# Kernel tuning notes

Measured on AMD Instinct MI355X. Metric: run time of the kernel, lower is better.

Reference implementation:

```python
import jax, jax.numpy as jnp
import numpy as np


def _relative_position_index(ws):
    # matches SpatialAttention.build with qWh=qWw=kWh=kWw=ws
    coords = np.stack(np.meshgrid(np.arange(ws), np.arange(ws), indexing='ij'))
    cf = coords.reshape(2, -1)  # [2, N]
    rel = (cf[:, :, None] - cf[:, None, :]).transpose(1, 2, 0)  # [N, N, 2]
    rel[:, :, 0] += ws - 1
    rel[:, :, 1] += ws - 1
    rel[:, :, 0] *= 2 * ws - 1
    return rel.sum(-1)  # [N, N] int in [0, (2*ws-1)^2)


def _shift_mask(H, W, ws, ss):
    # standard Swin shifted-window attention mask: [num_windows, N, N]
    img = np.zeros((H, W))
    cnt = 0
    for h in (slice(0, -ws), slice(-ws, -ss), slice(-ss, None)):
        for w in (slice(0, -ws), slice(-ws, -ss), slice(-ss, None)):
            img[h, w] = cnt
            cnt += 1
    win = img.reshape(H // ws, ws, W // ws, ws).transpose(0, 2, 1, 3).reshape(-1, ws * ws)
    diff = win[:, None, :] - win[:, :, None]
    return np.where(diff != 0, -100.0, 0.0).astype(np.float32)


def _window_partition(x, ws):
    B, H, W, C = x.shape
    x = x.reshape(B, H // ws, ws, W // ws, ws, C)
    x = x.transpose(0, 1, 3, 2, 4, 5)
    return x.reshape(-1, ws, ws, C)  # [B*nW, ws, ws, C]


def _window_reverse(x, ws, H, W):
    C = x.shape[-1]
    x = x.reshape(-1, H // ws, W // ws, ws, ws, C)
    x = x.transpose(0, 1, 3, 2, 4, 5)
    return x.reshape(-1, H, W, C)


def setup_inputs() -> dict:
    key = jax.random.key(0)
    k1, k2, k3, k4 = jax.random.split(key, 4)
    B, H, W, C = 16, 64, 64, 512
    num_heads, ws = 16, 8
    return {
        'q': jax.random.normal(k1, (B, H, W, C), dtype=jnp.float32),
        'k': jax.random.normal(k2, (B, H, W, C), dtype=jnp.float32),
        'v': jax.random.normal(k3, (B, H, W, C), dtype=jnp.float32),
        'bias_table': jax.random.normal(k4, ((2 * ws - 1) ** 2, num_heads), dtype=jnp.float32) * 0.02,
        'num_heads': num_heads,
        'window_size': ws,
        'shift_size': 4,
    }


def reference(q, k, v, bias_table, num_heads, window_size, shift_size):
    B, H, W, C = q.shape
    ws, ss = window_size, shift_size
    N = ws * ws
    hd = C // num_heads
    scale = hd ** -0.5

    # cyclic shift
    q = jnp.roll(q, (-ss, -ss), axis=(1, 2))
    k = jnp.roll(k, (-ss, -ss), axis=(1, 2))
    v = jnp.roll(v, (-ss, -ss), axis=(1, 2))

    # window partition -> [B*nW, heads, N, hd]
    def to_heads(x):
        x = _window_partition(x, ws).reshape(-1, N, num_heads, hd)
        return x.transpose(0, 2, 1, 3)

    qh, kh, vh = to_heads(q), to_heads(k), to_heads(v)

    attn = jnp.einsum('bhid,bhjd->bhij', qh * scale, kh)  # [BnW, h, N, N]

    # gathered relative position bias: [1, h, N, N]
    idx = jnp.asarray(_relative_position_index(ws))
    rel_bias = bias_table[idx.reshape(-1)].reshape(N, N, num_heads).transpose(2, 0, 1)
    attn = attn + rel_bias[None]

    # shifted-window mask: [nW, N, N]
    mask = jnp.asarray(_shift_mask(H, W, ws, ss))
    nW = mask.shape[0]
    attn = attn.reshape(-1, nW, num_heads, N, N) + mask[None, :, None]
    attn = attn.reshape(-1, num_heads, N, N)

    attn = jax.nn.softmax(attn, axis=-1)

    x = jnp.einsum('bhij,bhjd->bihd', attn, vh).reshape(-1, ws, ws, C)
    x = _window_reverse(x, ws, H, W)
    x = jnp.roll(x, (ss, ss), axis=(1, 2))  # reverse cyclic shift
    return x
```

## Files before the change

kernel.cpp:

```cpp
#include <hip/hip_runtime.h>

#define TB 16
#define NHEADS 16
#define HD 32
#define WS 8
#define SS 4
#define PPB 8

typedef __attribute__((ext_vector_type(8))) __bf16 bf16x8;
typedef __attribute__((ext_vector_type(4))) float f32x4;

#define OFF_Q 0
#define OFF_K 5120
#define OFF_P 0
#define OFF_V 10240

__global__ __launch_bounds__(256, 5)
void swin_attn_mfma(const float* __restrict__ q,
                    const float* __restrict__ k,
                    const float* __restrict__ v,
                    const float* __restrict__ bias_table,
                    float* __restrict__ out)
{
    __shared__ __align__(16) char smem[14848];
    char* sQ = smem + OFF_Q;
    char* sK = smem + OFF_K;
    char* sP = smem + OFF_P;
    char* sV = smem + OFF_V;

    const int beta = blockIdx.x;
    const int head = beta & (NHEADS - 1);
    const int wh   = (beta >> 4) & 7;
    const int b    = beta >> 7;

    const int tid  = threadIdx.x;
    const int wave = tid >> 6;
    const int lane = tid & 63;
    const int quad = lane >> 4, lm = lane & 15;
    const int ih = lane >> 3, iw = lane & 7;
    const int gh = (wh * WS + ih + SS) & 63;

    const int ihh  = 2 * wave + (quad >> 1);
    const int iww0 = 4 * (quad & 1);
    const int jw   = lm & 7;
    f32x4 bias[4];
    #pragma unroll
    for (int nt = 0; nt < 4; ++nt) {
        const int jh = 2 * nt + (lm >> 3);
        #pragma unroll
        for (int r = 0; r < 4; ++r)
            bias[nt][r] = bias_table[((ihh - jh + 7) * 15 + (iww0 + r - jw + 7)) * NHEADS + head];
    }
    const bool eh = (wh == 7);

    const float* base = (wave == 0) ? q : (wave == 1) ? k : v;
    const int t0 = (wave == 3) ? 4 : 0;
    const size_t rowpre = ((size_t)(b * 64 + gh)) * 64;

    float4 R[8];

    {
        const int gw = (iw + SS) & 63;
        const float4* src = (const float4*)(base + (rowpre + gw) * 512 + head * HD) + t0;
        R[0] = src[0]; R[1] = src[1]; R[2] = src[2]; R[3] = src[3];
        if (wave < 2) { R[4] = src[4]; R[5] = src[5]; R[6] = src[6]; R[7] = src[7]; }
    }

    for (int it = 0; it < PPB; ++it) {
        __syncthreads();

        if (wave == 0) {
            const float scale = 0.17677669529663687f;
            #pragma unroll
            for (int t = 0; t < 4; ++t) {
                float4 a = R[2 * t], c = R[2 * t + 1];
                bf16x8 w;
                w[0] = (__bf16)(a.x * scale); w[1] = (__bf16)(a.y * scale);
                w[2] = (__bf16)(a.z * scale); w[3] = (__bf16)(a.w * scale);
                w[4] = (__bf16)(c.x * scale); w[5] = (__bf16)(c.y * scale);
                w[6] = (__bf16)(c.z * scale); w[7] = (__bf16)(c.w * scale);
                *(bf16x8*)(sQ + lane * 80 + 16 * t) = w;
            }
        } else if (wave == 1) {
            #pragma unroll
            for (int t = 0; t < 4; ++t) {
                float4 a = R[2 * t], c = R[2 * t + 1];
                bf16x8 w;
                w[0] = (__bf16)a.x; w[1] = (__bf16)a.y;
                w[2] = (__bf16)a.z; w[3] = (__bf16)a.w;
                w[4] = (__bf16)c.x; w[5] = (__bf16)c.y;
                w[6] = (__bf16)c.z; w[7] = (__bf16)c.w;
                *(bf16x8*)(sK + lane * 80 + 16 * t) = w;
            }
        } else {
            #pragma unroll
            for (int t = 0; t < 4; ++t) {
                float4 x = R[t];
                const int ch = 4 * (t0 + t);
                *(__bf16*)(sV + (ch + 0) * 144 + lane * 2) = (__bf16)x.x;
                *(__bf16*)(sV + (ch + 1) * 144 + lane * 2) = (__bf16)x.y;
                *(__bf16*)(sV + (ch + 2) * 144 + lane * 2) = (__bf16)x.z;
                *(__bf16*)(sV + (ch + 3) * 144 + lane * 2) = (__bf16)x.w;
            }
        }

        if (it + 1 < PPB) {
            const int gw = ((it + 1) * WS + iw + SS) & 63;
            const float4* src = (const float4*)(base + (rowpre + gw) * 512 + head * HD) + t0;
            R[0] = src[0]; R[1] = src[1]; R[2] = src[2]; R[3] = src[3];
            if (wave < 2) { R[4] = src[4]; R[5] = src[5]; R[6] = src[6]; R[7] = src[7]; }
        }
        __syncthreads();

        bf16x8 qa = *(const bf16x8*)(sQ + (16 * wave + lm) * 80 + quad * 16);
        bf16x8 kb[4];
        #pragma unroll
        for (int nt = 0; nt < 4; ++nt)
            kb[nt] = *(const bf16x8*)(sK + (16 * nt + lm) * 80 + quad * 16);

        f32x4 S[4];
        #pragma unroll
        for (int nt = 0; nt < 4; ++nt) {
            f32x4 z = {0.f, 0.f, 0.f, 0.f};
            S[nt] = __builtin_amdgcn_mfma_f32_16x16x32_bf16(qa, kb[nt], z, 0, 0, 0);
        }

        const bool ew = (it == PPB - 1);
        float part[4] = {0.f, 0.f, 0.f, 0.f};
        #pragma unroll
        for (int nt = 0; nt < 4; ++nt) {
            const int jh = 2 * nt + (lm >> 3);
            const bool okh = !eh || ((ihh < 4) == (jh < 4));
            #pragma unroll
            for (int r = 0; r < 4; ++r) {
                const int iww = iww0 + r;
                float s = S[nt][r] + bias[nt][r];
                bool ok = okh && (!ew || ((iww < 4) == (jw < 4)));
                float e = ok ? __expf(s) : 0.f;
                S[nt][r] = e;
                part[r] += e;
            }
        }
        __syncthreads();

        #pragma unroll
        for (int nt = 0; nt < 4; ++nt)
            #pragma unroll
            for (int r = 0; r < 4; ++r)
                *(__bf16*)(sP + (16 * wave + 4 * quad + r) * 144 + (16 * nt + lm) * 2)
                    = (__bf16)S[nt][r];
        #pragma unroll
        for (int m = 1; m <= 8; m <<= 1)
            #pragma unroll
            for (int r = 0; r < 4; ++r)
                part[r] += __shfl_xor(part[r], m, 64);
        float rl[4];
        #pragma unroll
        for (int r = 0; r < 4; ++r)
            rl[r] = 1.f / part[r];
        __syncthreads();

        bf16x8 pa0 = *(const bf16x8*)(sP + (16 * wave + lm) * 144 + quad * 16);
        bf16x8 pa1 = *(const bf16x8*)(sP + (16 * wave + lm) * 144 + 64 + quad * 16);
        bf16x8 vb[2][2];
        #pragma unroll
        for (int nt = 0; nt < 2; ++nt)
            #pragma unroll
            for (int ks = 0; ks < 2; ++ks)
                vb[nt][ks] = *(const bf16x8*)(sV + (16 * nt + lm) * 144 + ks * 64 + quad * 16);

        f32x4 O[2];
        #pragma unroll
        for (int nt = 0; nt < 2; ++nt) {
            f32x4 z = {0.f, 0.f, 0.f, 0.f};
            z = __builtin_amdgcn_mfma_f32_16x16x32_bf16(pa0, vb[nt][0], z, 0, 0, 0);
            O[nt] = __builtin_amdgcn_mfma_f32_16x16x32_bf16(pa1, vb[nt][1], z, 0, 0, 0);
        }

        #pragma unroll
        for (int r = 0; r < 4; ++r) {
            const int i = 16 * wave + 4 * quad + r;
            const int ghh = (wh * WS + (i >> 3) + SS) & 63;
            const int gww = (it * WS + (i & 7) + SS) & 63;
            float* rp = out + (((size_t)b * 64 + ghh) * 64 + gww) * 512 + (size_t)head * HD + lm;
            rp[0]  = O[0][r] * rl[r];
            rp[16] = O[1][r] * rl[r];
        }
    }
}

extern "C" void kernel_launch(void* const* d_in, const int* in_sizes, int n_in,
                              void* d_out, int out_size, void* d_ws, size_t ws_size,
                              hipStream_t stream) {
    const float* q  = (const float*)d_in[0];
    const float* k  = (const float*)d_in[1];
    const float* v  = (const float*)d_in[2];
    const float* bt = (const float*)d_in[3];
    float* out = (float*)d_out;

    dim3 grid(TB * 64 * NHEADS / PPB);
    dim3 block(256);
    swin_attn_mfma<<<grid, block, 0, stream>>>(q, k, v, bt, out);
}
```

Baseline: 441.6 us.

## Process one window with four heads per block, loading all data upfront

```diff
diff --git a/kernel.cpp b/kernel.cpp
--- a/kernel.cpp
+++ b/kernel.cpp
@@ -5,118 +5,103 @@
 #define HD 32
 #define WS 8
 #define SS 4
-#define PPB 8
 
 typedef __attribute__((ext_vector_type(8))) __bf16 bf16x8;
+typedef __attribute__((ext_vector_type(4))) __bf16 bf16x4;
 typedef __attribute__((ext_vector_type(4))) float f32x4;
 
 #define OFF_Q 0
-#define OFF_K 5120
-#define OFF_P 0
-#define OFF_V 10240
+#define OFF_K 20480
+#define OFF_V 40960
+#define OFF_P 59392
+#define OFF_B 68608
 
-__global__ __launch_bounds__(256, 5)
+__global__ __launch_bounds__(256, 2)
 void swin_attn_mfma(const float* __restrict__ q,
                     const float* __restrict__ k,
                     const float* __restrict__ v,
                     const float* __restrict__ bias_table,
                     float* __restrict__ out)
 {
-    __shared__ __align__(16) char smem[14848];
-    char* sQ = smem + OFF_Q;
-    char* sK = smem + OFF_K;
+    __shared__ __align__(16) char smem[72208];
+    float* sB = (float*)(smem + OFF_B);
     char* sP = smem + OFF_P;
-    char* sV = smem + OFF_V;
 
-    const int beta = blockIdx.x;
-    const int head = beta & (NHEADS - 1);
-    const int wh   = (beta >> 4) & 7;
-    const int b    = beta >> 7;
+    const int blk = blockIdx.x;
+    const int hg  = blk & 3;
+    const int win = (blk >> 2) & 63;
+    const int b   = blk >> 8;
+    const int wh  = win >> 3;
+    const int ww  = win & 7;
 
     const int tid  = threadIdx.x;
     const int wave = tid >> 6;
     const int lane = tid & 63;
     const int quad = lane >> 4, lm = lane & 15;
-    const int ih = lane >> 3, iw = lane & 7;
-    const int gh = (wh * WS + ih + SS) & 63;
 
+    const int c4 = tid & 31;
+    const int tb = tid >> 5;
+    const int hs = c4 >> 3;
+    const int cw = c4 & 7;
+
+    if (tid < 225) {
+        #pragma unroll
+        for (int hl = 0; hl < 4; ++hl)
+            sB[hl * 225 + tid] = bias_table[tid * NHEADS + hg * 4 + hl];
+    }
+
+    {
+        const int gw = (ww * WS + tb + SS) & 63;
+        float4 RQ[8], RK[8], RV[8];
+        #pragma unroll
+        for (int it = 0; it < 8; ++it) {
+            const int gh = (wh * WS + it + SS) & 63;
+            const size_t f4 = (((size_t)(b * 64 + gh) * 64 + gw) * 128) + hg * 32 + c4;
+            RQ[it] = ((const float4*)q)[f4];
+            RK[it] = ((const float4*)k)[f4];
+            RV[it] = ((const float4*)v)[f4];
+        }
+        const float scale = 0.17677669529663687f;
+        #pragma unroll
+        for (int it = 0; it < 8; ++it) {
+            const int t = it * 8 + tb;
+            float4 a = RQ[it];
+            bf16x4 wq;
+            wq[0] = (__bf16)(a.x * scale); wq[1] = (__bf16)(a.y * scale);
+            wq[2] = (__bf16)(a.z * scale); wq[3] = (__bf16)(a.w * scale);
+            *(bf16x4*)(smem + OFF_Q + hs * 5120 + t * 80 + cw * 8) = wq;
+            float4 c = RK[it];
+            bf16x4 wk;
+            wk[0] = (__bf16)c.x; wk[1] = (__bf16)c.y;
+            wk[2] = (__bf16)c.z; wk[3] = (__bf16)c.w;
+            *(bf16x4*)(smem + OFF_K + hs * 5120 + t * 80 + cw * 8) = wk;
+            float4 d = RV[it];
+            char* vdst = smem + OFF_V + hs * 4608 + t * 2;
+            *(__bf16*)(vdst + (cw * 4 + 0) * 144) = (__bf16)d.x;
+            *(__bf16*)(vdst + (cw * 4 + 1) * 144) = (__bf16)d.y;
+            *(__bf16*)(vdst + (cw * 4 + 2) * 144) = (__bf16)d.z;
+            *(__bf16*)(vdst + (cw * 4 + 3) * 144) = (__bf16)d.w;
+        }
+    }
+    __syncthreads();
+
+    const bool eh = (wh == 7), ew = (ww == 7);
     const int ihh  = 2 * wave + (quad >> 1);
     const int iww0 = 4 * (quad & 1);
     const int jw   = lm & 7;
-    f32x4 bias[4];
+
     #pragma unroll
-    for (int nt = 0; nt < 4; ++nt) {
-        const int jh = 2 * nt + (lm >> 3);
-        #pragma unroll
-        for (int r = 0; r < 4; ++r)
-            bias[nt][r] = bias_table[((ihh - jh + 7) * 15 + (iww0 + r - jw + 7)) * NHEADS + head];
-    }
-    const bool eh = (wh == 7);
+    for (int hl = 0; hl < 4; ++hl) {
+        const char* sQh = smem + OFF_Q + hl * 5120;
+        const char* sKh = smem + OFF_K + hl * 5120;
+        const char* sVh = smem + OFF_V + hl * 4608;
+        const float* sBh = sB + hl * 225;
 
-    const float* base = (wave == 0) ? q : (wave == 1) ? k : v;
-    const int t0 = (wave == 3) ? 4 : 0;
-    const size_t rowpre = ((size_t)(b * 64 + gh)) * 64;
-
-    float4 R[8];
-
-    {
-        const int gw = (iw + SS) & 63;
-        const float4* src = (const float4*)(base + (rowpre + gw) * 512 + head * HD) + t0;
-        R[0] = src[0]; R[1] = src[1]; R[2] = src[2]; R[3] = src[3];
-        if (wave < 2) { R[4] = src[4]; R[5] = src[5]; R[6] = src[6]; R[7] = src[7]; }
-    }
-
-    for (int it = 0; it < PPB; ++it) {
-        __syncthreads();
-
-        if (wave == 0) {
-            const float scale = 0.17677669529663687f;
-            #pragma unroll
-            for (int t = 0; t < 4; ++t) {
-                float4 a = R[2 * t], c = R[2 * t + 1];
-                bf16x8 w;
-                w[0] = (__bf16)(a.x * scale); w[1] = (__bf16)(a.y * scale);
-                w[2] = (__bf16)(a.z * scale); w[3] = (__bf16)(a.w * scale);
-                w[4] = (__bf16)(c.x * scale); w[5] = (__bf16)(c.y * scale);
-                w[6] = (__bf16)(c.z * scale); w[7] = (__bf16)(c.w * scale);
-                *(bf16x8*)(sQ + lane * 80 + 16 * t) = w;
-            }
-        } else if (wave == 1) {
-            #pragma unroll
-            for (int t = 0; t < 4; ++t) {
-                float4 a = R[2 * t], c = R[2 * t + 1];
-                bf16x8 w;
-                w[0] = (__bf16)a.x; w[1] = (__bf16)a.y;
-                w[2] = (__bf16)a.z; w[3] = (__bf16)a.w;
-                w[4] = (__bf16)c.x; w[5] = (__bf16)c.y;
-                w[6] = (__bf16)c.z; w[7] = (__bf16)c.w;
-                *(bf16x8*)(sK + lane * 80 + 16 * t) = w;
-            }
-        } else {
-            #pragma unroll
-            for (int t = 0; t < 4; ++t) {
-                float4 x = R[t];
-                const int ch = 4 * (t0 + t);
-                *(__bf16*)(sV + (ch + 0) * 144 + lane * 2) = (__bf16)x.x;
-                *(__bf16*)(sV + (ch + 1) * 144 + lane * 2) = (__bf16)x.y;
-                *(__bf16*)(sV + (ch + 2) * 144 + lane * 2) = (__bf16)x.z;
-                *(__bf16*)(sV + (ch + 3) * 144 + lane * 2) = (__bf16)x.w;
-            }
-        }
-
-        if (it + 1 < PPB) {
-            const int gw = ((it + 1) * WS + iw + SS) & 63;
-            const float4* src = (const float4*)(base + (rowpre + gw) * 512 + head * HD) + t0;
-            R[0] = src[0]; R[1] = src[1]; R[2] = src[2]; R[3] = src[3];
-            if (wave < 2) { R[4] = src[4]; R[5] = src[5]; R[6] = src[6]; R[7] = src[7]; }
-        }
-        __syncthreads();
-
-        bf16x8 qa = *(const bf16x8*)(sQ + (16 * wave + lm) * 80 + quad * 16);
+        bf16x8 qa = *(const bf16x8*)(sQh + (16 * wave + lm) * 80 + quad * 16);
         bf16x8 kb[4];
         #pragma unroll
         for (int nt = 0; nt < 4; ++nt)
-            kb[nt] = *(const bf16x8*)(sK + (16 * nt + lm) * 80 + quad * 16);
+            kb[nt] = *(const bf16x8*)(sKh + (16 * nt + lm) * 80 + quad * 16);
 
         f32x4 S[4];
         #pragma unroll
@@ -125,7 +110,6 @@
             S[nt] = __builtin_amdgcn_mfma_f32_16x16x32_bf16(qa, kb[nt], z, 0, 0, 0);
         }
 
-        const bool ew = (it == PPB - 1);
         float part[4] = {0.f, 0.f, 0.f, 0.f};
         #pragma unroll
         for (int nt = 0; nt < 4; ++nt) {
@@ -134,14 +118,13 @@
             #pragma unroll
             for (int r = 0; r < 4; ++r) {
                 const int iww = iww0 + r;
-                float s = S[nt][r] + bias[nt][r];
+                float s = S[nt][r] + sBh[(ihh - jh + 7) * 15 + (iww + 7 - jw)];
                 bool ok = okh && (!ew || ((iww < 4) == (jw < 4)));
                 float e = ok ? __expf(s) : 0.f;
                 S[nt][r] = e;
                 part[r] += e;
             }
         }
-        __syncthreads();
 
         #pragma unroll
         for (int nt = 0; nt < 4; ++nt)
@@ -167,7 +150,7 @@
         for (int nt = 0; nt < 2; ++nt)
             #pragma unroll
             for (int ks = 0; ks < 2; ++ks)
-                vb[nt][ks] = *(const bf16x8*)(sV + (16 * nt + lm) * 144 + ks * 64 + quad * 16);
+                vb[nt][ks] = *(const bf16x8*)(sVh + (16 * nt + lm) * 144 + ks * 64 + quad * 16);
 
         f32x4 O[2];
         #pragma unroll
@@ -177,15 +160,17 @@
             O[nt] = __builtin_amdgcn_mfma_f32_16x16x32_bf16(pa1, vb[nt][1], z, 0, 0, 0);
         }
 
+        const int head = hg * 4 + hl;
         #pragma unroll
         for (int r = 0; r < 4; ++r) {
             const int i = 16 * wave + 4 * quad + r;
             const int ghh = (wh * WS + (i >> 3) + SS) & 63;
-            const int gww = (it * WS + (i & 7) + SS) & 63;
+            const int gww = (ww * WS + (i & 7) + SS) & 63;
             float* rp = out + (((size_t)b * 64 + ghh) * 64 + gww) * 512 + (size_t)head * HD + lm;
             rp[0]  = O[0][r] * rl[r];
             rp[16] = O[1][r] * rl[r];
         }
+        __syncthreads();
     }
 }
 
@@ -198,7 +183,7 @@
     const float* bt = (const float*)d_in[3];
     float* out = (float*)d_out;
 
-    dim3 grid(TB * 64 * NHEADS / PPB);
+    dim3 grid(TB * 64 * 4);
     dim3 block(256);
     swin_attn_mfma<<<grid, block, 0, stream>>>(q, k, v, bt, out);
 }
```

Measured after the change: 395.9 us. 1.12x faster.
